# Optimization experiments

Hardware: AMD Instinct MI355X
Metric: run time of the kernel (lower is better)

Reference implementation:

```python
import jax, jax.numpy as jnp
import numpy as np

N = 50000       # nodes
E = 100000      # edges (avg degree ~2 per direction, molecular graphs)
EDGE_DIM = 8
EH = 32         # edge-MLP hidden width
DIN = 32
H1, H2 = 32, 64
NGRAPH = 256
EPS = 1e-5


def setup_inputs():
    key = jax.random.key(0)
    ks = jax.random.split(key, 16)
    def rn(k, shape, fan):
        return jax.random.normal(k, shape, jnp.float32) * np.float32(1.0 / np.sqrt(fan))
    return {
        "x": jax.random.normal(ks[0], (N, DIN), jnp.float32),
        "edge_index": jax.random.randint(ks[1], (2, E), 0, N),
        "edge_attr": jax.random.uniform(ks[2], (E, EDGE_DIM), jnp.float32),
        "batch_index": jnp.sort(jax.random.randint(ks[3], (N,), 0, NGRAPH)),
        # NNConv layer 1: DIN -> H1
        "e1_w1": rn(ks[4], (EDGE_DIM, EH), EDGE_DIM), "e1_b1": jnp.zeros((EH,), jnp.float32),
        "e1_w2": rn(ks[5], (EH, DIN * H1), EH), "e1_b2": jnp.zeros((DIN * H1,), jnp.float32),
        "root1": rn(ks[6], (DIN, H1), DIN), "bias1": jnp.zeros((H1,), jnp.float32),
        # NNConv layer 2: H1 -> H2
        "e2_w1": rn(ks[7], (EDGE_DIM, EH), EDGE_DIM), "e2_b1": jnp.zeros((EH,), jnp.float32),
        "e2_w2": rn(ks[8], (EH, H1 * H2), EH), "e2_b2": jnp.zeros((H1 * H2,), jnp.float32),
        "root2": rn(ks[9], (H1, H2), H1), "bias2": jnp.zeros((H2,), jnp.float32),
        # MLP head
        "h1_w": rn(ks[10], (2 * H2, H2), 2 * H2), "h1_b": jnp.zeros((H2,), jnp.float32),
        "bn1_g": jnp.ones((H2,), jnp.float32), "bn1_b": jnp.zeros((H2,), jnp.float32),
        "bn1_m": jnp.zeros((H2,), jnp.float32), "bn1_v": jnp.ones((H2,), jnp.float32),
        "h2_w": rn(ks[11], (H2, H2 // 2), H2), "h2_b": jnp.zeros((H2 // 2,), jnp.float32),
        "bn2_g": jnp.ones((H2 // 2,), jnp.float32), "bn2_b": jnp.zeros((H2 // 2,), jnp.float32),
        "bn2_m": jnp.zeros((H2 // 2,), jnp.float32), "bn2_v": jnp.ones((H2 // 2,), jnp.float32),
        "h3_w": rn(ks[12], (H2 // 2, 1), H2 // 2), "h3_b": jnp.zeros((1,), jnp.float32),
    }


def nnconv_layer(x, src, dst, edge_attr, w1, b1, w2, b2, root, bias, din, dout):
    # edge MLP -> per-edge weight matrix [E, din, dout]
    h = jax.nn.relu(edge_attr @ w1 + b1)
    W = (h @ w2 + b2).reshape(-1, din, dout)
    # gather source features, per-edge matmul, scatter-add to targets
    msg = jnp.einsum('ei,eio->eo', x[src], W)
    agg = jax.ops.segment_sum(msg, dst, num_segments=x.shape[0])
    return x @ root + agg + bias


def bn_eval(x, g, b, m, v):
    return (x - m) * jax.lax.rsqrt(v + EPS) * g + b


def reference(x, edge_index, edge_attr, batch_index,
              e1_w1, e1_b1, e1_w2, e1_b2, root1, bias1,
              e2_w1, e2_b1, e2_w2, e2_b2, root2, bias2,
              h1_w, h1_b, bn1_g, bn1_b, bn1_m, bn1_v,
              h2_w, h2_b, bn2_g, bn2_b, bn2_m, bn2_v,
              h3_w, h3_b):
    src, dst = edge_index[0], edge_index[1]
    h = nnconv_layer(x, src, dst, edge_attr, e1_w1, e1_b1, e1_w2, e1_b2, root1, bias1, DIN, H1)
    h = jax.nn.relu(h)
    h = nnconv_layer(h, src, dst, edge_attr, e2_w1, e2_b1, e2_w2, e2_b2, root2, bias2, H1, H2)
    # global max + mean pool per graph
    gmax = jax.ops.segment_max(h, batch_index, num_segments=NGRAPH)
    cnt = jax.ops.segment_sum(jnp.ones((h.shape[0],), h.dtype), batch_index, num_segments=NGRAPH)
    gmean = jax.ops.segment_sum(h, batch_index, num_segments=NGRAPH) / jnp.maximum(cnt, 1.0)[:, None]
    feat = jnp.concatenate([gmax, gmean], axis=1)  # [NGRAPH, 2*H2]
    # MLP head (eval mode: BN uses running stats, dropout = identity)
    z = jax.nn.relu(bn_eval(feat @ h1_w + h1_b, bn1_g, bn1_b, bn1_m, bn1_v))
    z = jax.nn.relu(bn_eval(z @ h2_w + h2_b, bn2_g, bn2_b, bn2_m, bn2_v))
    return z @ h3_w + h3_b
```

## Files before the change

### kernel.cpp

```cpp
#include <hip/hip_runtime.h>
#include <hip/hip_fp16.h>

#define N_NODES 50000
#define N_EDGES 100000
#define EDGE_DIM 8
#define EHID 32
#define DIN 32
#define H1 32
#define H2 64
#define NGRAPH 256
#define BN_EPS 1e-5f
#define KTOT 1056

#define EH_BLOCKS  ((N_EDGES + 255) / 256)
#define PREP_TOTAL ((H1 + H2) * KTOT)
#define PREP_BLOCKS (PREP_TOTAL / 256)
#define INIT_BLOCKS 253
#define MSG_BLOCKS 512

typedef __attribute__((ext_vector_type(8))) _Float16 f16x8;
typedef __attribute__((ext_vector_type(4))) float f32x4;

__device__ inline void atomicMaxF(float* addr, float v) {
    if (v >= 0.0f) atomicMax((int*)addr, __float_as_int(v));
    else           atomicMin((unsigned int*)addr, __float_as_uint(v));
}

__device__ inline unsigned int pk_f16(float a, float b) {
    unsigned int r;
    asm("v_cvt_pkrtz_f16_f32 %0, %1, %2" : "=v"(r) : "v"(a), "v"(b));
    return r;
}

__global__ __launch_bounds__(256) void prologue_kernel(
    const float* __restrict__ edge_attr,
    const float* __restrict__ e1w1, const float* __restrict__ e1b1,
    const float* __restrict__ e2w1, const float* __restrict__ e2b1,
    const float* __restrict__ e1w2, const float* __restrict__ e1b2,
    const float* __restrict__ e2w2, const float* __restrict__ e2b2,
    unsigned int* __restrict__ hpk1, unsigned int* __restrict__ hpk2,
    unsigned short* __restrict__ w2h1, unsigned short* __restrict__ w2h2,
    float* __restrict__ agg1, float* __restrict__ agg2,
    float* __restrict__ gmax, float* __restrict__ gsum, float* __restrict__ gcnt)
{
    int bid = blockIdx.x, tid = threadIdx.x;
    if (bid < EH_BLOCKS) {
        __shared__ float s_w[2][EDGE_DIM * EHID];
        __shared__ float s_b[2][EHID];
        if (tid < EDGE_DIM * EHID) { s_w[0][tid] = e1w1[tid]; s_w[1][tid] = e2w1[tid]; }
        if (tid < EHID) { s_b[0][tid] = e1b1[tid]; s_b[1][tid] = e2b1[tid]; }
        __syncthreads();
        int e = bid * 256 + tid;
        if (e >= N_EDGES) return;
        const float4* eap = reinterpret_cast<const float4*>(edge_attr + (size_t)e * EDGE_DIM);
        float4 v0 = eap[0], v1 = eap[1];
        float ea[EDGE_DIM] = {v0.x, v0.y, v0.z, v0.w, v1.x, v1.y, v1.z, v1.w};
#pragma unroll
        for (int L = 0; L < 2; ++L) {
            unsigned int* hp = (L == 0 ? hpk1 : hpk2) + (size_t)e * EHID;
#pragma unroll
            for (int k4 = 0; k4 < EHID; k4 += 4) {
                unsigned int t[4];
#pragma unroll
                for (int q = 0; q < 4; ++q) {
                    int k = k4 + q;
                    float acc = s_b[L][k];
#pragma unroll
                    for (int j = 0; j < EDGE_DIM; ++j) acc += ea[j] * s_w[L][j * EHID + k];
                    acc = fmaxf(acc, 0.0f);
                    t[q] = pk_f16(acc, acc);
                }
                uint4 r; r.x = t[0]; r.y = t[1]; r.z = t[2]; r.w = t[3];
                *reinterpret_cast<uint4*>(hp + k4) = r;
            }
        }
    } else if (bid < EH_BLOCKS + PREP_BLOCKS) {
        int idx = (bid - EH_BLOCKS) * 256 + tid;
        const int n1 = H1 * KTOT;
        if (idx < n1) {
            int o = idx / KTOT, k = idx % KTOT;
            float v = (k < EHID * DIN) ? e1w2[(k >> 5) * (DIN * H1) + (k & 31) * H1 + o]
                                       : e1b2[(k - EHID * DIN) * H1 + o];
            w2h1[idx] = __half_as_ushort(__float2half(v));
        } else {
            int j = idx - n1;
            int o = j / KTOT, k = j % KTOT;
            float v = (k < EHID * DIN) ? e2w2[(k >> 5) * (DIN * H2) + (k & 31) * H2 + o]
                                       : e2b2[(k - EHID * DIN) * H2 + o];
            w2h2[j] = __half_as_ushort(__float2half(v));
        }
    } else {
        int lb = bid - EH_BLOCKS - PREP_BLOCKS;
        int stride = INIT_BLOCKS * 256;
        int i0 = lb * 256 + tid;
        for (int i = i0; i < N_NODES * H1; i += stride) agg1[i] = 0.0f;
        for (int i = i0; i < N_NODES * H2; i += stride) agg2[i] = 0.0f;
        for (int i = i0; i < NGRAPH * H2; i += stride) { gmax[i] = __int_as_float(0xff800000); gsum[i] = 0.0f; }
        for (int i = i0; i < NGRAPH; i += stride) gcnt[i] = 0.0f;
    }
}

template <int DOUT>
__global__ __launch_bounds__(256, 2) void msg_v3_kernel(
    const float* __restrict__ gsrc,
    const unsigned int* __restrict__ hpk,
    const int* __restrict__ src, const int* __restrict__ dst,
    const unsigned short* __restrict__ w2h,
    float* __restrict__ agg)
{
    constexpr int NT = DOUT / 16;
    __shared__ unsigned int hlds[4][16][33];

    const int tid = threadIdx.x;
    const int wave = tid >> 6;
    const int lane = tid & 63;
    const int col = lane & 15;
    const int kq = lane >> 4;

    const int wg = blockIdx.x * 4 + wave;
    const int ot = wg & (NT - 1);
    const int stream = wg / NT;
    const int nstreams = (MSG_BLOCKS * 4) / NT;

    f16x8 B[33];
    {
        const unsigned short* bp = w2h + (size_t)(ot * 16 + col) * KTOT + kq * 8;
#pragma unroll
        for (int kk = 0; kk < 33; ++kk)
            B[kk] = *reinterpret_cast<const f16x8*>(bp + kk * 32);
    }

    const int nchunks = N_EDGES / 16;
    for (int c = stream; c < nchunks; c += nstreams) {
        const int e0 = c * 16;
        const int myE = e0 + col;
        const int s = src[myE];

        float4 ga = *reinterpret_cast<const float4*>(gsrc + (size_t)s * DIN + kq * 8);
        float4 gb = *reinterpret_cast<const float4*>(gsrc + (size_t)s * DIN + kq * 8 + 4);
        union { unsigned int u[4]; f16x8 v; } gf;
        gf.u[0] = pk_f16(ga.x, ga.y);
        gf.u[1] = pk_f16(ga.z, ga.w);
        gf.u[2] = pk_f16(gb.x, gb.y);
        gf.u[3] = pk_f16(gb.z, gb.w);

        const uint4* hp = reinterpret_cast<const uint4*>(hpk + (size_t)myE * EHID + kq * 8);
        uint4 h0 = hp[0], h1v = hp[1];
        *reinterpret_cast<uint4*>(&hlds[wave][col][kq * 8]) = h0;
        *reinterpret_cast<uint4*>(&hlds[wave][col][kq * 8 + 4]) = h1v;
        asm volatile("s_waitcnt lgkmcnt(0)" ::: "memory");

        f32x4 acc = (f32x4){0.f, 0.f, 0.f, 0.f};
#pragma unroll
        for (int kk = 0; kk < 32; ++kk) {
            unsigned int hh = hlds[wave][col][kk];
            union { unsigned int u[4]; f16x8 v; } af;
            asm("v_pk_mul_f16 %0, %1, %2" : "=v"(af.u[0]) : "v"(hh), "v"(gf.u[0]));
            asm("v_pk_mul_f16 %0, %1, %2" : "=v"(af.u[1]) : "v"(hh), "v"(gf.u[1]));
            asm("v_pk_mul_f16 %0, %1, %2" : "=v"(af.u[2]) : "v"(hh), "v"(gf.u[2]));
            asm("v_pk_mul_f16 %0, %1, %2" : "=v"(af.u[3]) : "v"(hh), "v"(gf.u[3]));
            acc = __builtin_amdgcn_mfma_f32_16x16x32_f16(af.v, B[kk], acc, 0, 0, 0);
        }
        acc = __builtin_amdgcn_mfma_f32_16x16x32_f16(gf.v, B[32], acc, 0, 0, 0);

        int4 dd = *reinterpret_cast<const int4*>(dst + e0 + kq * 4);
        const int dv[4] = {dd.x, dd.y, dd.z, dd.w};
#pragma unroll
        for (int r = 0; r < 4; ++r)
            atomicAdd(&agg[(size_t)dv[r] * DOUT + ot * 16 + col], acc[r]);
    }
}

template <int DOUTN, bool RELU>
__global__ __launch_bounds__(256) void node_update_kernel(
    const float* __restrict__ in, const float* __restrict__ root,
    const float* __restrict__ agg, const float* __restrict__ bias,
    float* __restrict__ out)
{
    constexpr int NPB = 256 / DOUTN;
    __shared__ float roots[DIN * DOUTN];
    __shared__ float ins[NPB][DIN + 1];
    int tid = threadIdx.x;
    for (int idx = tid; idx < DIN * DOUTN; idx += 256) roots[idx] = root[idx];
    int o = tid % DOUTN, nl = tid / DOUTN;
    float bo = bias[o];
    const int nchunks = (N_NODES + NPB - 1) / NPB;
    for (int c = blockIdx.x; c < nchunks; c += gridDim.x) {
        int nBase = c * NPB;
        __syncthreads();
        for (int idx = tid; idx < NPB * DIN; idx += 256) {
            int nn = nBase + idx / DIN;
            ins[idx / DIN][idx % DIN] = (nn < N_NODES) ? in[(size_t)nn * DIN + (idx % DIN)] : 0.0f;
        }
        __syncthreads();
        int n = nBase + nl;
        if (n < N_NODES) {
            float t = agg[(size_t)n * DOUTN + o] + bo;
#pragma unroll
            for (int i = 0; i < DIN; ++i) t += ins[nl][i] * roots[i * DOUTN + o];
            if (RELU) t = fmaxf(t, 0.0f);
            out[(size_t)n * DOUTN + o] = t;
        }
    }
}

__global__ __launch_bounds__(256) void pool_scan_kernel(
    const float* __restrict__ h, const int* __restrict__ batch,
    float* gmax, float* gsum, float* gcnt)
{
    __shared__ int s_batch[64];
    int tid = threadIdx.x;
    int base = blockIdx.x * 64;
    if (tid < 64) s_batch[tid] = (base + tid < N_NODES) ? batch[base + tid] : -1;
    __syncthreads();
    int o = tid & 63, r = tid >> 6;
    int curb = -1; float s = 0.f, m = __int_as_float(0xff800000); float c = 0.f;
#pragma unroll
    for (int j = 0; j < 16; ++j) {
        int n = base + r * 16 + j;
        if (n >= N_NODES) break;
        int b = s_batch[r * 16 + j];
        if (b != curb) {
            if (curb >= 0) {
                atomicAdd(&gsum[curb * H2 + o], s);
                atomicMaxF(&gmax[curb * H2 + o], m);
                if (o == 0) atomicAdd(&gcnt[curb], c);
            }
            curb = b; s = 0.f; m = __int_as_float(0xff800000); c = 0.f;
        }
        float v = h[(size_t)n * H2 + o];
        s += v; m = fmaxf(m, v); c += 1.f;
    }
    if (curb >= 0) {
        atomicAdd(&gsum[curb * H2 + o], s);
        atomicMaxF(&gmax[curb * H2 + o], m);
        if (o == 0) atomicAdd(&gcnt[curb], c);
    }
}

__global__ __launch_bounds__(128) void head_kernel(
    const float* __restrict__ gmax, const float* __restrict__ gsum, const float* __restrict__ gcnt,
    const float* __restrict__ h1w, const float* __restrict__ h1b,
    const float* __restrict__ bn1g, const float* __restrict__ bn1b,
    const float* __restrict__ bn1m, const float* __restrict__ bn1v,
    const float* __restrict__ h2w, const float* __restrict__ h2b,
    const float* __restrict__ bn2g, const float* __restrict__ bn2b,
    const float* __restrict__ bn2m, const float* __restrict__ bn2v,
    const float* __restrict__ h3w, const float* __restrict__ h3b,
    float* __restrict__ out)
{
    __shared__ float feat[2 * H2];
    __shared__ float z1s[H2];
    __shared__ float z2s[H2 / 2];
    int b = blockIdx.x, tid = threadIdx.x;
    float cnt = fmaxf(gcnt[b], 1.0f);
    if (tid < H2) feat[tid] = gmax[b * H2 + tid];
    else          feat[tid] = gsum[b * H2 + (tid - H2)] / cnt;
    __syncthreads();
    if (tid < H2) {
        float acc = h1b[tid];
#pragma unroll
        for (int j = 0; j < 2 * H2; ++j) acc += feat[j] * h1w[j * H2 + tid];
        acc = (acc - bn1m[tid]) * rsqrtf(bn1v[tid] + BN_EPS) * bn1g[tid] + bn1b[tid];
        z1s[tid] = fmaxf(acc, 0.0f);
    }
    __syncthreads();
    if (tid < H2 / 2) {
        float acc = h2b[tid];
#pragma unroll
        for (int j = 0; j < H2; ++j) acc += z1s[j] * h2w[j * (H2 / 2) + tid];
        acc = (acc - bn2m[tid]) * rsqrtf(bn2v[tid] + BN_EPS) * bn2g[tid] + bn2b[tid];
        z2s[tid] = fmaxf(acc, 0.0f);
    }
    __syncthreads();
    if (tid == 0) {
        float acc = h3b[0];
#pragma unroll
        for (int j = 0; j < H2 / 2; ++j) acc += z2s[j] * h3w[j];
        out[b] = acc;
    }
}

extern "C" void kernel_launch(void* const* d_in, const int* in_sizes, int n_in,
                              void* d_out, int out_size, void* d_ws, size_t ws_size,
                              hipStream_t stream)
{
    const float* x         = (const float*)d_in[0];
    const int*   ei        = (const int*)d_in[1];
    const float* edge_attr = (const float*)d_in[2];
    const int*   batch     = (const int*)d_in[3];
    const float* e1_w1 = (const float*)d_in[4];
    const float* e1_b1 = (const float*)d_in[5];
    const float* e1_w2 = (const float*)d_in[6];
    const float* e1_b2 = (const float*)d_in[7];
    const float* root1 = (const float*)d_in[8];
    const float* bias1 = (const float*)d_in[9];
    const float* e2_w1 = (const float*)d_in[10];
    const float* e2_b1 = (const float*)d_in[11];
    const float* e2_w2 = (const float*)d_in[12];
    const float* e2_b2 = (const float*)d_in[13];
    const float* root2 = (const float*)d_in[14];
    const float* bias2 = (const float*)d_in[15];
    const float* h1w = (const float*)d_in[16];
    const float* h1b = (const float*)d_in[17];
    const float* bn1g = (const float*)d_in[18];
    const float* bn1b = (const float*)d_in[19];
    const float* bn1m = (const float*)d_in[20];
    const float* bn1v = (const float*)d_in[21];
    const float* h2w = (const float*)d_in[22];
    const float* h2b = (const float*)d_in[23];
    const float* bn2g = (const float*)d_in[24];
    const float* bn2b = (const float*)d_in[25];
    const float* bn2m = (const float*)d_in[26];
    const float* bn2v = (const float*)d_in[27];
    const float* h3w = (const float*)d_in[28];
    const float* h3b = (const float*)d_in[29];
    float* out = (float*)d_out;

    float* ws = (float*)d_ws;
    unsigned int* hpk1 = (unsigned int*)ws;
    unsigned int* hpk2 = hpk1 + (size_t)N_EDGES * EHID;
    float* out1  = (float*)(hpk2 + (size_t)N_EDGES * EHID);
    float* agg1  = out1 + (size_t)N_NODES * H1;
    float* agg2  = agg1 + (size_t)N_NODES * H1;
    float* gmaxb = agg2 + (size_t)N_NODES * H2;
    float* gsumb = gmaxb + NGRAPH * H2;
    float* gcntb = gsumb + NGRAPH * H2;
    unsigned short* w2h1 = (unsigned short*)(gcntb + 256);
    unsigned short* w2h2 = w2h1 + (size_t)H1 * KTOT;
    float* h2o = (float*)hpk1;

    const int* srcp = ei;
    const int* dstp = ei + N_EDGES;

    prologue_kernel<<<EH_BLOCKS + PREP_BLOCKS + INIT_BLOCKS, 256, 0, stream>>>(
        edge_attr, e1_w1, e1_b1, e2_w1, e2_b1, e1_w2, e1_b2, e2_w2, e2_b2,
        hpk1, hpk2, w2h1, w2h2, agg1, agg2, gmaxb, gsumb, gcntb);

    msg_v3_kernel<H1><<<MSG_BLOCKS, 256, 0, stream>>>(x, hpk1, srcp, dstp, w2h1, agg1);
    node_update_kernel<H1, true><<<2048, 256, 0, stream>>>(x, root1, agg1, bias1, out1);

    msg_v3_kernel<H2><<<MSG_BLOCKS, 256, 0, stream>>>(out1, hpk2, srcp, dstp, w2h2, agg2);
    node_update_kernel<H2, false><<<2048, 256, 0, stream>>>(out1, root2, agg2, bias2, h2o);

    pool_scan_kernel<<<(N_NODES + 63) / 64, 256, 0, stream>>>(h2o, batch, gmaxb, gsumb, gcntb);
    head_kernel<<<NGRAPH, 128, 0, stream>>>(gmaxb, gsumb, gcntb,
                                            h1w, h1b, bn1g, bn1b, bn1m, bn1v,
                                            h2w, h2b, bn2g, bn2b, bn2m, bn2v,
                                            h3w, h3b, out);
}
```

Baseline: 122.2 us.

## Software-pipeline message kernel with double-buffered LDS and two interleaved edge tiles

```diff
diff --git a/kernel.cpp b/kernel.cpp
--- a/kernel.cpp
+++ b/kernel.cpp
@@ -20,16 +20,28 @@
 
 typedef __attribute__((ext_vector_type(8))) _Float16 f16x8;
 typedef __attribute__((ext_vector_type(4))) float f32x4;
+typedef unsigned int uint32;
 
 __device__ inline void atomicMaxF(float* addr, float v) {
     if (v >= 0.0f) atomicMax((int*)addr, __float_as_int(v));
     else           atomicMin((unsigned int*)addr, __float_as_uint(v));
 }
 
-__device__ inline unsigned int pk_f16(float a, float b) {
-    unsigned int r;
+__device__ inline uint32 pk_f16(float a, float b) {
+    uint32 r;
     asm("v_cvt_pkrtz_f16_f32 %0, %1, %2" : "=v"(r) : "v"(a), "v"(b));
     return r;
+}
+
+union GF { uint32 u[4]; f16x8 v; };
+
+__device__ inline f16x8 mul_h(uint32 h, const GF& g) {
+    GF r;
+    asm("v_pk_mul_f16 %0, %1, %2" : "=v"(r.u[0]) : "v"(h), "v"(g.u[0]));
+    asm("v_pk_mul_f16 %0, %1, %2" : "=v"(r.u[1]) : "v"(h), "v"(g.u[1]));
+    asm("v_pk_mul_f16 %0, %1, %2" : "=v"(r.u[2]) : "v"(h), "v"(g.u[2]));
+    asm("v_pk_mul_f16 %0, %1, %2" : "=v"(r.u[3]) : "v"(h), "v"(g.u[3]));
+    return r.v;
 }
 
 __global__ __launch_bounds__(256) void prologue_kernel(
@@ -38,7 +50,7 @@
     const float* __restrict__ e2w1, const float* __restrict__ e2b1,
     const float* __restrict__ e1w2, const float* __restrict__ e1b2,
     const float* __restrict__ e2w2, const float* __restrict__ e2b2,
-    unsigned int* __restrict__ hpk1, unsigned int* __restrict__ hpk2,
+    uint32* __restrict__ hpk1, uint32* __restrict__ hpk2,
     unsigned short* __restrict__ w2h1, unsigned short* __restrict__ w2h2,
     float* __restrict__ agg1, float* __restrict__ agg2,
     float* __restrict__ gmax, float* __restrict__ gsum, float* __restrict__ gcnt)
@@ -57,10 +69,10 @@
         float ea[EDGE_DIM] = {v0.x, v0.y, v0.z, v0.w, v1.x, v1.y, v1.z, v1.w};
 #pragma unroll
         for (int L = 0; L < 2; ++L) {
-            unsigned int* hp = (L == 0 ? hpk1 : hpk2) + (size_t)e * EHID;
+            uint32* hp = (L == 0 ? hpk1 : hpk2) + (size_t)e * EHID;
 #pragma unroll
             for (int k4 = 0; k4 < EHID; k4 += 4) {
-                unsigned int t[4];
+                uint32 t[4];
 #pragma unroll
                 for (int q = 0; q < 4; ++q) {
                     int k = k4 + q;
@@ -101,15 +113,15 @@
 }
 
 template <int DOUT>
-__global__ __launch_bounds__(256, 2) void msg_v3_kernel(
+__global__ __launch_bounds__(256, 2) void msg_v4_kernel(
     const float* __restrict__ gsrc,
-    const unsigned int* __restrict__ hpk,
+    const uint32* __restrict__ hpk,
     const int* __restrict__ src, const int* __restrict__ dst,
     const unsigned short* __restrict__ w2h,
     float* __restrict__ agg)
 {
     constexpr int NT = DOUT / 16;
-    __shared__ unsigned int hlds[4][16][33];
+    __shared__ __align__(16) uint32 hlds[4][2][32][36];
 
     const int tid = threadIdx.x;
     const int wave = tid >> 6;
@@ -117,10 +129,11 @@
     const int col = lane & 15;
     const int kq = lane >> 4;
 
-    const int wg = blockIdx.x * 4 + wave;
-    const int ot = wg & (NT - 1);
-    const int stream = wg / NT;
-    const int nstreams = (MSG_BLOCKS * 4) / NT;
+    const int w = blockIdx.x * 4 + wave;
+    const int ot = w % NT;
+    int it = w / NT;
+    const int strideIt = (MSG_BLOCKS * 4) / NT;
+    const int NIT = N_EDGES / 32;
 
     f16x8 B[33];
     {
@@ -129,45 +142,101 @@
         for (int kk = 0; kk < 33; ++kk)
             B[kk] = *reinterpret_cast<const f16x8*>(bp + kk * 32);
     }
-
-    const int nchunks = N_EDGES / 16;
-    for (int c = stream; c < nchunks; c += nstreams) {
-        const int e0 = c * 16;
-        const int myE = e0 + col;
-        const int s = src[myE];
-
-        float4 ga = *reinterpret_cast<const float4*>(gsrc + (size_t)s * DIN + kq * 8);
-        float4 gb = *reinterpret_cast<const float4*>(gsrc + (size_t)s * DIN + kq * 8 + 4);
-        union { unsigned int u[4]; f16x8 v; } gf;
-        gf.u[0] = pk_f16(ga.x, ga.y);
-        gf.u[1] = pk_f16(ga.z, ga.w);
-        gf.u[2] = pk_f16(gb.x, gb.y);
-        gf.u[3] = pk_f16(gb.z, gb.w);
-
-        const uint4* hp = reinterpret_cast<const uint4*>(hpk + (size_t)myE * EHID + kq * 8);
-        uint4 h0 = hp[0], h1v = hp[1];
-        *reinterpret_cast<uint4*>(&hlds[wave][col][kq * 8]) = h0;
-        *reinterpret_cast<uint4*>(&hlds[wave][col][kq * 8 + 4]) = h1v;
-        asm volatile("s_waitcnt lgkmcnt(0)" ::: "memory");
-
-        f32x4 acc = (f32x4){0.f, 0.f, 0.f, 0.f};
-#pragma unroll
-        for (int kk = 0; kk < 32; ++kk) {
-            unsigned int hh = hlds[wave][col][kk];
-            union { unsigned int u[4]; f16x8 v; } af;
-            asm("v_pk_mul_f16 %0, %1, %2" : "=v"(af.u[0]) : "v"(hh), "v"(gf.u[0]));
-            asm("v_pk_mul_f16 %0, %1, %2" : "=v"(af.u[1]) : "v"(hh), "v"(gf.u[1]));
-            asm("v_pk_mul_f16 %0, %1, %2" : "=v"(af.u[2]) : "v"(hh), "v"(gf.u[2]));
-            asm("v_pk_mul_f16 %0, %1, %2" : "=v"(af.u[3]) : "v"(hh), "v"(gf.u[3]));
-            acc = __builtin_amdgcn_mfma_f32_16x16x32_f16(af.v, B[kk], acc, 0, 0, 0);
-        }
-        acc = __builtin_amdgcn_mfma_f32_16x16x32_f16(gf.v, B[32], acc, 0, 0, 0);
-
-        int4 dd = *reinterpret_cast<const int4*>(dst + e0 + kq * 4);
-        const int dv[4] = {dd.x, dd.y, dd.z, dd.w};
-#pragma unroll
-        for (int r = 0; r < 4; ++r)
-            atomicAdd(&agg[(size_t)dv[r] * DOUT + ot * 16 + col], acc[r]);
+    if (it >= NIT) return;
+
+    int buf = 0;
+
+    int e0 = it * 32;
+    int sA = src[e0 + col], sB = src[e0 + 16 + col];
+    float4 gA0 = *reinterpret_cast<const float4*>(gsrc + (size_t)sA * DIN + kq * 8);
+    float4 gA1 = *reinterpret_cast<const float4*>(gsrc + (size_t)sA * DIN + kq * 8 + 4);
+    float4 gB0 = *reinterpret_cast<const float4*>(gsrc + (size_t)sB * DIN + kq * 8);
+    float4 gB1 = *reinterpret_cast<const float4*>(gsrc + (size_t)sB * DIN + kq * 8 + 4);
+    uint4 hA0 = *reinterpret_cast<const uint4*>(hpk + (size_t)(e0 + col) * EHID + kq * 8);
+    uint4 hA1 = *reinterpret_cast<const uint4*>(hpk + (size_t)(e0 + col) * EHID + kq * 8 + 4);
+    uint4 hB0 = *reinterpret_cast<const uint4*>(hpk + (size_t)(e0 + 16 + col) * EHID + kq * 8);
+    uint4 hB1 = *reinterpret_cast<const uint4*>(hpk + (size_t)(e0 + 16 + col) * EHID + kq * 8 + 4);
+    int4 ddA = *reinterpret_cast<const int4*>(dst + e0 + kq * 4);
+    int4 ddB = *reinterpret_cast<const int4*>(dst + e0 + 16 + kq * 4);
+
+    int it1 = it + strideIt;
+    int s1A = 0, s1B = 0;
+    if (it1 < NIT) { s1A = src[it1 * 32 + col]; s1B = src[it1 * 32 + 16 + col]; }
+
+    GF gfA, gfB;
+    gfA.u[0] = pk_f16(gA0.x, gA0.y); gfA.u[1] = pk_f16(gA0.z, gA0.w);
+    gfA.u[2] = pk_f16(gA1.x, gA1.y); gfA.u[3] = pk_f16(gA1.z, gA1.w);
+    gfB.u[0] = pk_f16(gB0.x, gB0.y); gfB.u[1] = pk_f16(gB0.z, gB0.w);
+    gfB.u[2] = pk_f16(gB1.x, gB1.y); gfB.u[3] = pk_f16(gB1.z, gB1.w);
+    *reinterpret_cast<uint4*>(&hlds[wave][0][col][kq * 8])          = hA0;
+    *reinterpret_cast<uint4*>(&hlds[wave][0][col][kq * 8 + 4])      = hA1;
+    *reinterpret_cast<uint4*>(&hlds[wave][0][16 + col][kq * 8])     = hB0;
+    *reinterpret_cast<uint4*>(&hlds[wave][0][16 + col][kq * 8 + 4]) = hB1;
+
+    for (;;) {
+        int it2 = it1 + strideIt;
+        int s2A = 0, s2B = 0;
+        if (it2 < NIT) { s2A = src[it2 * 32 + col]; s2B = src[it2 * 32 + 16 + col]; }
+
+        const bool nv = (it1 < NIT);
+        float4 ngA0, ngA1, ngB0, ngB1;
+        uint4 nhA0, nhA1, nhB0, nhB1;
+        int4 nddA, nddB;
+        if (nv) {
+            int ne0 = it1 * 32;
+            ngA0 = *reinterpret_cast<const float4*>(gsrc + (size_t)s1A * DIN + kq * 8);
+            ngA1 = *reinterpret_cast<const float4*>(gsrc + (size_t)s1A * DIN + kq * 8 + 4);
+            ngB0 = *reinterpret_cast<const float4*>(gsrc + (size_t)s1B * DIN + kq * 8);
+            ngB1 = *reinterpret_cast<const float4*>(gsrc + (size_t)s1B * DIN + kq * 8 + 4);
+            nhA0 = *reinterpret_cast<const uint4*>(hpk + (size_t)(ne0 + col) * EHID + kq * 8);
+            nhA1 = *reinterpret_cast<const uint4*>(hpk + (size_t)(ne0 + col) * EHID + kq * 8 + 4);
+            nhB0 = *reinterpret_cast<const uint4*>(hpk + (size_t)(ne0 + 16 + col) * EHID + kq * 8);
+            nhB1 = *reinterpret_cast<const uint4*>(hpk + (size_t)(ne0 + 16 + col) * EHID + kq * 8 + 4);
+            nddA = *reinterpret_cast<const int4*>(dst + ne0 + kq * 4);
+            nddB = *reinterpret_cast<const int4*>(dst + ne0 + 16 + kq * 4);
+        }
+
+        f32x4 accA = (f32x4){0.f, 0.f, 0.f, 0.f};
+        f32x4 accB = (f32x4){0.f, 0.f, 0.f, 0.f};
+#pragma unroll
+        for (int t = 0; t < 8; ++t) {
+            uint4 ha = *reinterpret_cast<const uint4*>(&hlds[wave][buf][col][t * 4]);
+            uint4 hb = *reinterpret_cast<const uint4*>(&hlds[wave][buf][16 + col][t * 4]);
+            accA = __builtin_amdgcn_mfma_f32_16x16x32_f16(mul_h(ha.x, gfA), B[t * 4 + 0], accA, 0, 0, 0);
+            accB = __builtin_amdgcn_mfma_f32_16x16x32_f16(mul_h(hb.x, gfB), B[t * 4 + 0], accB, 0, 0, 0);
+            accA = __builtin_amdgcn_mfma_f32_16x16x32_f16(mul_h(ha.y, gfA), B[t * 4 + 1], accA, 0, 0, 0);
+            accB = __builtin_amdgcn_mfma_f32_16x16x32_f16(mul_h(hb.y, gfB), B[t * 4 + 1], accB, 0, 0, 0);
+            accA = __builtin_amdgcn_mfma_f32_16x16x32_f16(mul_h(ha.z, gfA), B[t * 4 + 2], accA, 0, 0, 0);
+            accB = __builtin_amdgcn_mfma_f32_16x16x32_f16(mul_h(hb.z, gfB), B[t * 4 + 2], accB, 0, 0, 0);
+            accA = __builtin_amdgcn_mfma_f32_16x16x32_f16(mul_h(ha.w, gfA), B[t * 4 + 3], accA, 0, 0, 0);
+            accB = __builtin_amdgcn_mfma_f32_16x16x32_f16(mul_h(hb.w, gfB), B[t * 4 + 3], accB, 0, 0, 0);
+        }
+        accA = __builtin_amdgcn_mfma_f32_16x16x32_f16(gfA.v, B[32], accA, 0, 0, 0);
+        accB = __builtin_amdgcn_mfma_f32_16x16x32_f16(gfB.v, B[32], accB, 0, 0, 0);
+
+        atomicAdd(&agg[(size_t)ddA.x * DOUT + ot * 16 + col], accA[0]);
+        atomicAdd(&agg[(size_t)ddA.y * DOUT + ot * 16 + col], accA[1]);
+        atomicAdd(&agg[(size_t)ddA.z * DOUT + ot * 16 + col], accA[2]);
+        atomicAdd(&agg[(size_t)ddA.w * DOUT + ot * 16 + col], accA[3]);
+        atomicAdd(&agg[(size_t)ddB.x * DOUT + ot * 16 + col], accB[0]);
+        atomicAdd(&agg[(size_t)ddB.y * DOUT + ot * 16 + col], accB[1]);
+        atomicAdd(&agg[(size_t)ddB.z * DOUT + ot * 16 + col], accB[2]);
+        atomicAdd(&agg[(size_t)ddB.w * DOUT + ot * 16 + col], accB[3]);
+
+        if (!nv) break;
+
+        buf ^= 1;
+        *reinterpret_cast<uint4*>(&hlds[wave][buf][col][kq * 8])          = nhA0;
+        *reinterpret_cast<uint4*>(&hlds[wave][buf][col][kq * 8 + 4])      = nhA1;
+        *reinterpret_cast<uint4*>(&hlds[wave][buf][16 + col][kq * 8])     = nhB0;
+        *reinterpret_cast<uint4*>(&hlds[wave][buf][16 + col][kq * 8 + 4]) = nhB1;
+        gfA.u[0] = pk_f16(ngA0.x, ngA0.y); gfA.u[1] = pk_f16(ngA0.z, ngA0.w);
+        gfA.u[2] = pk_f16(ngA1.x, ngA1.y); gfA.u[3] = pk_f16(ngA1.z, ngA1.w);
+        gfB.u[0] = pk_f16(ngB0.x, ngB0.y); gfB.u[1] = pk_f16(ngB0.z, ngB0.w);
+        gfB.u[2] = pk_f16(ngB1.x, ngB1.y); gfB.u[3] = pk_f16(ngB1.z, ngB1.w);
+        ddA = nddA; ddB = nddB;
+        s1A = s2A; s1B = s2B;
+        it = it1; it1 = it2;
     }
 }
 
@@ -318,8 +387,8 @@
     float* out = (float*)d_out;
 
     float* ws = (float*)d_ws;
-    unsigned int* hpk1 = (unsigned int*)ws;
-    unsigned int* hpk2 = hpk1 + (size_t)N_EDGES * EHID;
+    uint32* hpk1 = (uint32*)ws;
+    uint32* hpk2 = hpk1 + (size_t)N_EDGES * EHID;
     float* out1  = (float*)(hpk2 + (size_t)N_EDGES * EHID);
     float* agg1  = out1 + (size_t)N_NODES * H1;
     float* agg2  = agg1 + (size_t)N_NODES * H1;
@@ -337,10 +406,10 @@
         edge_attr, e1_w1, e1_b1, e2_w1, e2_b1, e1_w2, e1_b2, e2_w2, e2_b2,
         hpk1, hpk2, w2h1, w2h2, agg1, agg2, gmaxb, gsumb, gcntb);
 
-    msg_v3_kernel<H1><<<MSG_BLOCKS, 256, 0, stream>>>(x, hpk1, srcp, dstp, w2h1, agg1);
+    msg_v4_kernel<H1><<<MSG_BLOCKS, 256, 0, stream>>>(x, hpk1, srcp, dstp, w2h1, agg1);
     node_update_kernel<H1, true><<<2048, 256, 0, stream>>>(x, root1, agg1, bias1, out1);
 
-    msg_v3_kernel<H2><<<MSG_BLOCKS, 256, 0, stream>>>(out1, hpk2, srcp, dstp, w2h2, agg2);
+    msg_v4_kernel<H2><<<MSG_BLOCKS, 256, 0, stream>>>(out1, hpk2, srcp, dstp, w2h2, agg2);
     node_update_kernel<H2, false><<<2048, 256, 0, stream>>>(out1, root2, agg2, bias2, h2o);
 
     pool_scan_kernel<<<(N_NODES + 63) / 64, 256, 0, stream>>>(h2o, batch, gmaxb, gsumb, gcntb);
```

Measured after the change: 116.9 us. -4.3%, faster.
